# Performance work log

Measured on AMD Instinct MI355X. Metric: run time of the kernel, lower is better.

Reference implementation:

```python
import jax, jax.numpy as jnp
import numpy as np

NUM_EMBEDDINGS = 512
EMBEDDING_DIM = 64


def setup_inputs() -> dict:
    key = jax.random.key(0)
    k_in, k_emb = jax.random.split(key)
    inputs = jax.random.normal(k_in, (8, 64, 16, 32, 32), dtype=jnp.float32)
    # matches torch uniform_(-1/K, 1/K) init
    lim = 1.0 / NUM_EMBEDDINGS
    embedding = jax.random.uniform(
        k_emb, (NUM_EMBEDDINGS, EMBEDDING_DIM), dtype=jnp.float32,
        minval=-lim, maxval=lim)
    return {"inputs": inputs, "embedding": embedding}


def reference(inputs, embedding):
    # inputs: (B, C=D, T, H, W); embedding: (K, D)
    x = jnp.transpose(inputs, (0, 2, 3, 4, 1))  # (B, T, H, W, D)
    in_shape = x.shape
    flat = x.reshape(-1, EMBEDDING_DIM)  # (N, D)
    distances = (
        jnp.sum(flat * flat, axis=1, keepdims=True)
        + jnp.sum(embedding * embedding, axis=1)
        - 2.0 * jnp.matmul(flat, embedding.T)
    )  # (N, K)
    # NOTE: original applies softmax to raw (positive) distances, faithfully kept
    weights = jax.nn.softmax(distances, axis=1)
    out = jnp.matmul(weights, embedding).reshape(in_shape)  # (B,T,H,W,D)
    return jnp.transpose(out, (0, 4, 1, 2, 3))  # (B, D, T, H, W)
```

## Files before the change

### kernel.cpp

```cpp
#include <hip/hip_runtime.h>
#include <hip/hip_bf16.h>

typedef __attribute__((ext_vector_type(8))) short short8;
typedef __attribute__((ext_vector_type(4))) short short4v;
typedef __attribute__((ext_vector_type(8))) _Float16 half8;
typedef __attribute__((ext_vector_type(2))) __fp16 fp16x2;
typedef __attribute__((ext_vector_type(4))) float f32x4;

#define SPW 16384
#define XST 72
#define RW  67
#define LOG2E 1.4426950408889634f

__device__ __forceinline__ float exp2_hw(float f) {
  return __builtin_amdgcn_exp2f(f);
}

__device__ __forceinline__ short bf16s(float f) {
  union { __hip_bfloat16 h; short s; } u;
  u.h = __float2bfloat16(f);
  return u.s;
}

__global__ void prep_all(const float* __restrict__ emb, short8* __restrict__ a1b,
                         half8* __restrict__ eb3, float* __restrict__ norms) {
  const int f = blockIdx.x * 256 + threadIdx.x;
  if (f < 4096) {
    const int s = f & 1;
    const int lane = (f >> 1) & 63;
    const int kt = f >> 7;
    const int row = kt * 16 + (lane & 15);
    const int col0 = s * 32 + (lane >> 4) * 8;
    short8 v;
    #pragma unroll
    for (int i = 0; i < 8; ++i)
      v[i] = bf16s(-2.0f * LOG2E * emb[row * 64 + col0 + i]);
    a1b[f] = v;
  } else if (f < 8192) {
    const int e = f - 4096;
    const int m2 = e & 3;
    const int lane = (e >> 2) & 63;
    const int pr = e >> 8;
    const int g = lane >> 4;
    const int d = m2 * 16 + (lane & 15);
    half8 v;
    #pragma unroll
    for (int i = 0; i < 8; ++i) {
      const int k = (i < 4) ? (pr * 32 + 4 * g + i) : (pr * 32 + 16 + 4 * g + (i - 4));
      v[i] = (_Float16)emb[k * 64 + d];
    }
    eb3[e] = v;
  } else if (f < 8704) {
    const int k = f - 8192;
    float acc = 0.f;
    #pragma unroll
    for (int d = 0; d < 64; ++d) { float e = emb[k * 64 + d]; acc += e * e; }
    norms[k] = acc * LOG2E;
  }
}

__global__ __launch_bounds__(256, 3) void vq_main(
    const float* __restrict__ x, const short8* __restrict__ a1b,
    const half8* __restrict__ eb3, const float* __restrict__ norms,
    float* __restrict__ out) {
  __shared__ __align__(16) char lds_raw[35840];
  short* Xl   = reinterpret_cast<short*>(lds_raw);
  float* Rf   = reinterpret_cast<float*>(lds_raw);
  float* denl = reinterpret_cast<float*>(lds_raw + 34304);
  float* rden = reinterpret_cast<float*>(lds_raw + 35328);

  const int t = threadIdx.x;
  const int lane = t & 63;
  const int w = t >> 6;
  const int cg = w & 1;
  const int kg = w >> 1;
  const int l15 = lane & 15;
  const int g = lane >> 4;

  const int tile = blockIdx.x * 128;
  const int b = tile >> 14;
  const int off = tile & 16383;
  const float* xb = x + (size_t)b * (64 * SPW) + off;
  float* ob = out + (size_t)b * (64 * SPW) + off;

  {
    const int n0 = 4 * (t & 15);
    const int d0 = 4 * (t >> 4);
    #pragma unroll
    for (int h = 0; h < 2; ++h) {
      const int nb = h * 64 + n0;
      const float4 r0 = *reinterpret_cast<const float4*>(xb + (size_t)(d0 + 0) * SPW + nb);
      const float4 r1 = *reinterpret_cast<const float4*>(xb + (size_t)(d0 + 1) * SPW + nb);
      const float4 r2 = *reinterpret_cast<const float4*>(xb + (size_t)(d0 + 2) * SPW + nb);
      const float4 r3 = *reinterpret_cast<const float4*>(xb + (size_t)(d0 + 3) * SPW + nb);
      const short4v c0 = {bf16s(r0.x), bf16s(r1.x), bf16s(r2.x), bf16s(r3.x)};
      const short4v c1 = {bf16s(r0.y), bf16s(r1.y), bf16s(r2.y), bf16s(r3.y)};
      const short4v c2 = {bf16s(r0.z), bf16s(r1.z), bf16s(r2.z), bf16s(r3.z)};
      const short4v c3 = {bf16s(r0.w), bf16s(r1.w), bf16s(r2.w), bf16s(r3.w)};
      *reinterpret_cast<short4v*>(&Xl[(nb + 0) * XST + d0]) = c0;
      *reinterpret_cast<short4v*>(&Xl[(nb + 1) * XST + d0]) = c1;
      *reinterpret_cast<short4v*>(&Xl[(nb + 2) * XST + d0]) = c2;
      *reinterpret_cast<short4v*>(&Xl[(nb + 3) * XST + d0]) = c3;
    }
  }
  __syncthreads();

  short8 bx[4][2];
  #pragma unroll
  for (int j = 0; j < 4; ++j) {
    const int base = (cg * 64 + j * 16 + l15) * XST + g * 8;
    bx[j][0] = *reinterpret_cast<const short8*>(&Xl[base]);
    bx[j][1] = *reinterpret_cast<const short8*>(&Xl[base + 32]);
  }
  __syncthreads();

  f32x4 pacc[4][4];
  #pragma unroll
  for (int j = 0; j < 4; ++j)
    #pragma unroll
    for (int m2 = 0; m2 < 4; ++m2) pacc[j][m2] = f32x4{0.f, 0.f, 0.f, 0.f};
  float denp[4] = {0.f, 0.f, 0.f, 0.f};

  #pragma unroll
  for (int p = 0; p < 8; ++p) {
    const int pr = kg * 8 + p;
    const int ktA = pr * 2;
    const short8* ap = &a1b[(ktA * 64 + lane) * 2];
    const short8 aA0 = ap[0];
    const short8 aA1 = ap[1];
    const short8 aB0 = ap[128];
    const short8 aB1 = ap[129];
    const half8* ep = &eb3[(pr * 64 + lane) * 4];
    const half8 e0 = ep[0];
    const half8 e1 = ep[1];
    const half8 e2 = ep[2];
    const half8 e3 = ep[3];
    const float4 nvA = *reinterpret_cast<const float4*>(&norms[ktA * 16 + g * 4]);
    const float4 nvB = *reinterpret_cast<const float4*>(&norms[ktA * 16 + 16 + g * 4]);

    #pragma unroll
    for (int j = 0; j < 4; ++j) {
      f32x4 zA = {nvA.x, nvA.y, nvA.z, nvA.w};
      zA = __builtin_amdgcn_mfma_f32_16x16x32_bf16(aA0, bx[j][0], zA, 0, 0, 0);
      zA = __builtin_amdgcn_mfma_f32_16x16x32_bf16(aA1, bx[j][1], zA, 0, 0, 0);
      f32x4 zB = {nvB.x, nvB.y, nvB.z, nvB.w};
      zB = __builtin_amdgcn_mfma_f32_16x16x32_bf16(aB0, bx[j][0], zB, 0, 0, 0);
      zB = __builtin_amdgcn_mfma_f32_16x16x32_bf16(aB1, bx[j][1], zB, 0, 0, 0);
      const float p0 = exp2_hw(zA[0]);
      const float p1 = exp2_hw(zA[1]);
      const float p2 = exp2_hw(zA[2]);
      const float p3 = exp2_hw(zA[3]);
      const float p4 = exp2_hw(zB[0]);
      const float p5 = exp2_hw(zB[1]);
      const float p6 = exp2_hw(zB[2]);
      const float p7 = exp2_hw(zB[3]);
      denp[j] += ((p0 + p1) + (p2 + p3)) + ((p4 + p5) + (p6 + p7));
      union { fp16x2 h2[4]; half8 h8; } pk;
      pk.h2[0] = __builtin_amdgcn_cvt_pkrtz(p0, p1);
      pk.h2[1] = __builtin_amdgcn_cvt_pkrtz(p2, p3);
      pk.h2[2] = __builtin_amdgcn_cvt_pkrtz(p4, p5);
      pk.h2[3] = __builtin_amdgcn_cvt_pkrtz(p6, p7);
      const half8 pa = pk.h8;
      pacc[j][0] = __builtin_amdgcn_mfma_f32_16x16x32_f16(pa, e0, pacc[j][0], 0, 0, 0);
      pacc[j][1] = __builtin_amdgcn_mfma_f32_16x16x32_f16(pa, e1, pacc[j][1], 0, 0, 0);
      pacc[j][2] = __builtin_amdgcn_mfma_f32_16x16x32_f16(pa, e2, pacc[j][2], 0, 0, 0);
      pacc[j][3] = __builtin_amdgcn_mfma_f32_16x16x32_f16(pa, e3, pacc[j][3], 0, 0, 0);
    }
  }

  #pragma unroll
  for (int j = 0; j < 4; ++j) {
    denp[j] += __shfl_xor(denp[j], 16, 64);
    denp[j] += __shfl_xor(denp[j], 32, 64);
  }
  if (lane < 16) {
    #pragma unroll
    for (int j = 0; j < 4; ++j)
      denl[kg * 128 + cg * 64 + j * 16 + l15] = denp[j];
  }

  if (kg == 0) {
    #pragma unroll
    for (int j = 0; j < 4; ++j)
      #pragma unroll
      for (int m2 = 0; m2 < 4; ++m2)
        #pragma unroll
        for (int r = 0; r < 4; ++r)
          Rf[(cg * 64 + j * 16 + 4 * g + r) * RW + m2 * 16 + l15] = pacc[j][m2][r];
  }
  __syncthreads();

  if (kg == 1) {
    #pragma unroll
    for (int j = 0; j < 4; ++j)
      #pragma unroll
      for (int m2 = 0; m2 < 4; ++m2)
        #pragma unroll
        for (int r = 0; r < 4; ++r)
          Rf[(cg * 64 + j * 16 + 4 * g + r) * RW + m2 * 16 + l15] += pacc[j][m2][r];
  } else {
    rden[t & 127] = 1.0f / (denl[t & 127] + denl[128 + (t & 127)]);
  }
  __syncthreads();

  const int nq = t & 31;
  const int n = 4 * nq;
  const int dh = t >> 5;
  #pragma unroll
  for (int it = 0; it < 8; ++it) {
    const int d = it * 8 + dh;
    const float4 o = {Rf[(n + 0) * RW + d] * rden[n + 0],
                      Rf[(n + 1) * RW + d] * rden[n + 1],
                      Rf[(n + 2) * RW + d] * rden[n + 2],
                      Rf[(n + 3) * RW + d] * rden[n + 3]};
    *reinterpret_cast<float4*>(&ob[(size_t)d * SPW + n]) = o;
  }
}

extern "C" void kernel_launch(void* const* d_in, const int* in_sizes, int n_in,
                              void* d_out, int out_size, void* d_ws, size_t ws_size,
                              hipStream_t stream) {
  (void)in_sizes; (void)n_in; (void)out_size; (void)ws_size;
  const float* x   = (const float*)d_in[0];
  const float* emb = (const float*)d_in[1];
  float* out = (float*)d_out;

  char* ws = (char*)d_ws;
  short8* a1b  = (short8*)ws;
  half8*  eb3  = (half8*)(ws + 65536);
  float*  norms = (float*)(ws + 131072);

  prep_all<<<34, 256, 0, stream>>>(emb, a1b, eb3, norms);
  vq_main<<<1024, 256, 0, stream>>>(x, a1b, eb3, norms, out);
}
```

Measured before the change: 46.63 us.

## Double-buffer codebook fragments and compute softmax denominators via MFMA with ones

Embedding, codebook and norm fragments are now loaded into two alternating register sets, so the next pair's global loads overlap the current pair's MFMA work. The per-row softmax denominator is computed with an extra f16 MFMA against a ones vector instead of scalar adds plus cross-lane shuffles. Launch bounds drop from 3 to 2 waves per SIMD to allow more registers for the extra buffers. The denominator now sums fp16-rounded probabilities rather than fp32 values, and lower occupancy may reduce latency hiding.

```diff
diff --git a/kernel.cpp b/kernel.cpp
--- a/kernel.cpp
+++ b/kernel.cpp
@@ -59,7 +59,70 @@
   }
 }
 
-__global__ __launch_bounds__(256, 3) void vq_main(
+struct Frags {
+  short8 aA0, aA1, aB0, aB1;
+  half8 e0, e1, e2, e3;
+  float4 nvA, nvB;
+};
+
+__device__ __forceinline__ void ldfrag(Frags& f, const short8* __restrict__ a1b,
+                                       const half8* __restrict__ eb3,
+                                       const float* __restrict__ norms,
+                                       int pr, int lane, int g) {
+  const int ktA = pr * 2;
+  f.nvA = *reinterpret_cast<const float4*>(&norms[ktA * 16 + g * 4]);
+  f.nvB = *reinterpret_cast<const float4*>(&norms[ktA * 16 + 16 + g * 4]);
+  const short8* ap = &a1b[(ktA * 64 + lane) * 2];
+  f.aA0 = ap[0];
+  f.aA1 = ap[1];
+  f.aB0 = ap[128];
+  f.aB1 = ap[129];
+  const half8* ep = &eb3[(pr * 64 + lane) * 4];
+  f.e0 = ep[0];
+  f.e1 = ep[1];
+  f.e2 = ep[2];
+  f.e3 = ep[3];
+}
+
+__device__ __forceinline__ half8 make_pa(float p0, float p1, float p2, float p3,
+                                         float p4, float p5, float p6, float p7) {
+  const unsigned a = __builtin_bit_cast(unsigned, __builtin_amdgcn_cvt_pkrtz(p0, p1));
+  const unsigned b = __builtin_bit_cast(unsigned, __builtin_amdgcn_cvt_pkrtz(p2, p3));
+  const unsigned c = __builtin_bit_cast(unsigned, __builtin_amdgcn_cvt_pkrtz(p4, p5));
+  const unsigned d = __builtin_bit_cast(unsigned, __builtin_amdgcn_cvt_pkrtz(p6, p7));
+  const uint4 u = {a, b, c, d};
+  return __builtin_bit_cast(half8, u);
+}
+
+__device__ __forceinline__ void compute_unit(const Frags& f, const short8 bx[4][2],
+                                             f32x4 pacc[4][4], f32x4 dacc[4],
+                                             const half8 ones) {
+  #pragma unroll
+  for (int j = 0; j < 4; ++j) {
+    f32x4 zA = {f.nvA.x, f.nvA.y, f.nvA.z, f.nvA.w};
+    zA = __builtin_amdgcn_mfma_f32_16x16x32_bf16(f.aA0, bx[j][0], zA, 0, 0, 0);
+    zA = __builtin_amdgcn_mfma_f32_16x16x32_bf16(f.aA1, bx[j][1], zA, 0, 0, 0);
+    f32x4 zB = {f.nvB.x, f.nvB.y, f.nvB.z, f.nvB.w};
+    zB = __builtin_amdgcn_mfma_f32_16x16x32_bf16(f.aB0, bx[j][0], zB, 0, 0, 0);
+    zB = __builtin_amdgcn_mfma_f32_16x16x32_bf16(f.aB1, bx[j][1], zB, 0, 0, 0);
+    const float p0 = exp2_hw(zA[0]);
+    const float p1 = exp2_hw(zA[1]);
+    const float p2 = exp2_hw(zA[2]);
+    const float p3 = exp2_hw(zA[3]);
+    const float p4 = exp2_hw(zB[0]);
+    const float p5 = exp2_hw(zB[1]);
+    const float p6 = exp2_hw(zB[2]);
+    const float p7 = exp2_hw(zB[3]);
+    const half8 pa = make_pa(p0, p1, p2, p3, p4, p5, p6, p7);
+    pacc[j][0] = __builtin_amdgcn_mfma_f32_16x16x32_f16(pa, f.e0, pacc[j][0], 0, 0, 0);
+    pacc[j][1] = __builtin_amdgcn_mfma_f32_16x16x32_f16(pa, f.e1, pacc[j][1], 0, 0, 0);
+    pacc[j][2] = __builtin_amdgcn_mfma_f32_16x16x32_f16(pa, f.e2, pacc[j][2], 0, 0, 0);
+    pacc[j][3] = __builtin_amdgcn_mfma_f32_16x16x32_f16(pa, f.e3, pacc[j][3], 0, 0, 0);
+    dacc[j] = __builtin_amdgcn_mfma_f32_16x16x32_f16(pa, ones, dacc[j], 0, 0, 0);
+  }
+}
+
+__global__ __launch_bounds__(256, 2) void vq_main(
     const float* __restrict__ x, const short8* __restrict__ a1b,
     const half8* __restrict__ eb3, const float* __restrict__ norms,
     float* __restrict__ out) {
@@ -119,64 +182,29 @@
   for (int j = 0; j < 4; ++j)
     #pragma unroll
     for (int m2 = 0; m2 < 4; ++m2) pacc[j][m2] = f32x4{0.f, 0.f, 0.f, 0.f};
-  float denp[4] = {0.f, 0.f, 0.f, 0.f};
-
-  #pragma unroll
-  for (int p = 0; p < 8; ++p) {
-    const int pr = kg * 8 + p;
-    const int ktA = pr * 2;
-    const short8* ap = &a1b[(ktA * 64 + lane) * 2];
-    const short8 aA0 = ap[0];
-    const short8 aA1 = ap[1];
-    const short8 aB0 = ap[128];
-    const short8 aB1 = ap[129];
-    const half8* ep = &eb3[(pr * 64 + lane) * 4];
-    const half8 e0 = ep[0];
-    const half8 e1 = ep[1];
-    const half8 e2 = ep[2];
-    const half8 e3 = ep[3];
-    const float4 nvA = *reinterpret_cast<const float4*>(&norms[ktA * 16 + g * 4]);
-    const float4 nvB = *reinterpret_cast<const float4*>(&norms[ktA * 16 + 16 + g * 4]);
-
-    #pragma unroll
-    for (int j = 0; j < 4; ++j) {
-      f32x4 zA = {nvA.x, nvA.y, nvA.z, nvA.w};
-      zA = __builtin_amdgcn_mfma_f32_16x16x32_bf16(aA0, bx[j][0], zA, 0, 0, 0);
-      zA = __builtin_amdgcn_mfma_f32_16x16x32_bf16(aA1, bx[j][1], zA, 0, 0, 0);
-      f32x4 zB = {nvB.x, nvB.y, nvB.z, nvB.w};
-      zB = __builtin_amdgcn_mfma_f32_16x16x32_bf16(aB0, bx[j][0], zB, 0, 0, 0);
-      zB = __builtin_amdgcn_mfma_f32_16x16x32_bf16(aB1, bx[j][1], zB, 0, 0, 0);
-      const float p0 = exp2_hw(zA[0]);
-      const float p1 = exp2_hw(zA[1]);
-      const float p2 = exp2_hw(zA[2]);
-      const float p3 = exp2_hw(zA[3]);
-      const float p4 = exp2_hw(zB[0]);
-      const float p5 = exp2_hw(zB[1]);
-      const float p6 = exp2_hw(zB[2]);
-      const float p7 = exp2_hw(zB[3]);
-      denp[j] += ((p0 + p1) + (p2 + p3)) + ((p4 + p5) + (p6 + p7));
-      union { fp16x2 h2[4]; half8 h8; } pk;
-      pk.h2[0] = __builtin_amdgcn_cvt_pkrtz(p0, p1);
-      pk.h2[1] = __builtin_amdgcn_cvt_pkrtz(p2, p3);
-      pk.h2[2] = __builtin_amdgcn_cvt_pkrtz(p4, p5);
-      pk.h2[3] = __builtin_amdgcn_cvt_pkrtz(p6, p7);
-      const half8 pa = pk.h8;
-      pacc[j][0] = __builtin_amdgcn_mfma_f32_16x16x32_f16(pa, e0, pacc[j][0], 0, 0, 0);
-      pacc[j][1] = __builtin_amdgcn_mfma_f32_16x16x32_f16(pa, e1, pacc[j][1], 0, 0, 0);
-      pacc[j][2] = __builtin_amdgcn_mfma_f32_16x16x32_f16(pa, e2, pacc[j][2], 0, 0, 0);
-      pacc[j][3] = __builtin_amdgcn_mfma_f32_16x16x32_f16(pa, e3, pacc[j][3], 0, 0, 0);
-    }
-  }
-
-  #pragma unroll
-  for (int j = 0; j < 4; ++j) {
-    denp[j] += __shfl_xor(denp[j], 16, 64);
-    denp[j] += __shfl_xor(denp[j], 32, 64);
-  }
-  if (lane < 16) {
+  f32x4 dacc[4];
+  #pragma unroll
+  for (int j = 0; j < 4; ++j) dacc[j] = f32x4{0.f, 0.f, 0.f, 0.f};
+  const half8 ones = {(_Float16)1.f, (_Float16)1.f, (_Float16)1.f, (_Float16)1.f,
+                      (_Float16)1.f, (_Float16)1.f, (_Float16)1.f, (_Float16)1.f};
+
+  const int prb = kg * 8;
+  Frags fA, fB;
+  ldfrag(fA, a1b, eb3, norms, prb + 0, lane, g);
+  #pragma unroll
+  for (int p2 = 0; p2 < 4; ++p2) {
+    ldfrag(fB, a1b, eb3, norms, prb + 2 * p2 + 1, lane, g);
+    compute_unit(fA, bx, pacc, dacc, ones);
+    if (p2 < 3) ldfrag(fA, a1b, eb3, norms, prb + 2 * p2 + 2, lane, g);
+    compute_unit(fB, bx, pacc, dacc, ones);
+  }
+
+  if (l15 == 0) {
     #pragma unroll
     for (int j = 0; j < 4; ++j)
-      denl[kg * 128 + cg * 64 + j * 16 + l15] = denp[j];
+      #pragma unroll
+      for (int r = 0; r < 4; ++r)
+        denl[kg * 128 + cg * 64 + j * 16 + 4 * g + r] = dacc[j][r];
   }
 
   if (kg == 0) {
```

Result: faster. 38.03 us (-18.5%).
